# Performance work log

Measured on AMD Instinct MI355X. Metric: run time of the kernel, lower is better.

## Reference

```python
import jax, jax.numpy as jnp
import numpy as np
from jax import lax

D_MODEL = 1024
D_FF = 4096
NUM_EXPERTS = 24
TOP_K = 2
B, S = 2, 2048


def setup_inputs() -> dict:
    key = jax.random.key(0)
    ks = jax.random.split(key, 5)
    x = jax.random.normal(ks[0], (B, S, D_MODEL), dtype=jnp.float32)
    gate_w = jax.random.normal(ks[1], (D_MODEL, NUM_EXPERTS), dtype=jnp.float32) * 0.02
    gate_b = jnp.zeros((NUM_EXPERTS,), dtype=jnp.float32)
    w1 = jax.random.normal(ks[2], (NUM_EXPERTS, D_MODEL, D_FF), dtype=jnp.float32) * 0.02
    b1 = jnp.zeros((NUM_EXPERTS, D_FF), dtype=jnp.float32)
    w2 = jax.random.normal(ks[3], (NUM_EXPERTS, D_FF, D_MODEL), dtype=jnp.float32) * 0.02
    b2 = jnp.zeros((NUM_EXPERTS, D_MODEL), dtype=jnp.float32)
    return {"x": x, "gate_w": gate_w, "gate_b": gate_b,
            "w1": w1, "b1": b1, "w2": w2, "b2": b2}


def reference(x, gate_w, gate_b, w1, b1, w2, b2):
    b, s, d = x.shape
    t = b * s
    xf = x.reshape(t, d)  # [T, d]
    scores = xf @ gate_w + gate_b  # [T, E]
    top_val, top_idx = lax.top_k(scores, TOP_K)  # [T, k]
    prob = jax.nn.softmax(top_val, axis=-1)  # softmax over the top-k logits
    # scatter top-k probabilities into dense per-expert combine weights [T, E]
    combine = jnp.zeros((t, NUM_EXPERTS), dtype=x.dtype)
    combine = combine.at[jnp.arange(t)[:, None], top_idx].add(prob)

    def body(acc, expert):
        w1e, b1e, w2e, b2e, ce = expert  # ce: [T]
        h = jax.nn.gelu(xf @ w1e + b1e, approximate=False)  # exact GELU as torch default
        y = h @ w2e + b2e  # [T, d]
        return acc + ce[:, None] * y, None

    out, _ = lax.scan(body, jnp.zeros_like(xf), (w1, b1, w2, b2, combine.T))
    return out.reshape(b, s, d)
```

## Files before the change

kernel.cpp:

```cpp
#include <hip/hip_runtime.h>
#include <math.h>

#define DM 1024
#define DF 4096
#define NE 24
#define T_TOK 4096
#define T2 (T_TOK*2)

#define BM 128
#define BN 128
#define BK 64
#define MTILES 8
#define NK1 (DM / BK)
#define NK2H (DF / BK / 2)

typedef __attribute__((ext_vector_type(4))) float f32x4;
typedef __attribute__((ext_vector_type(2))) float f32x2;
typedef __attribute__((ext_vector_type(8))) short s16x8;

static __device__ __forceinline__ unsigned short f2bf(float f) {
    unsigned int u = __float_as_uint(f);
    unsigned int r = u + 0x7fffu + ((u >> 16) & 1u);
    return (unsigned short)(r >> 16);
}

static __device__ __forceinline__ unsigned int cvtpk(float lo, float hi) {
    unsigned int r;
    asm("v_cvt_pk_bf16_f32 %0, %1, %2" : "=v"(r) : "v"(lo), "v"(hi));
    return r;
}

#define GLL(gsrc, ldst)                                                          \
    __builtin_amdgcn_global_load_lds(                                            \
        (const __attribute__((address_space(1))) void*)(gsrc),                   \
        (__attribute__((address_space(3))) void*)(ldst), 16, 0, 0)


__global__ void k_transpose_gw(const float* __restrict__ gw, float* __restrict__ gwT) {
    int e = blockIdx.x;
    for (int d = threadIdx.x; d < DM; d += blockDim.x)
        gwT[e * DM + d] = gw[d * NE + e];
}

__global__ void k_gate(const float* __restrict__ x, const float* __restrict__ gwT,
                       const float* __restrict__ gb,
                       int* __restrict__ idx, float* __restrict__ prob) {
    int wave = threadIdx.x >> 6;
    int lane = threadIdx.x & 63;
    int t = blockIdx.x * 4 + wave;
    if (t >= T_TOK) return;
    const float* xr = x + (size_t)t * DM;
    float acc[NE];
#pragma unroll
    for (int e = 0; e < NE; e++) acc[e] = 0.f;
    for (int i = 0; i < DM / 64; i++) {
        int d = lane + i * 64;
        float xv = xr[d];
#pragma unroll
        for (int e = 0; e < NE; e++) acc[e] = fmaf(xv, gwT[e * DM + d], acc[e]);
    }
#pragma unroll
    for (int e = 0; e < NE; e++) {
        float v = acc[e];
        for (int off = 32; off >= 1; off >>= 1) v += __shfl_xor(v, off);
        acc[e] = v;
    }
    if (lane == 0) {
        float v1 = -1e30f, v2 = -1e30f;
        int i1 = -1, i2 = -1;
        for (int e = 0; e < NE; e++) {
            float s = acc[e] + gb[e];
            if (s > v1) { v2 = v1; i2 = i1; v1 = s; i1 = e; }
            else if (s > v2) { v2 = s; i2 = e; }
        }
        float e2 = expf(v2 - v1);
        float inv = 1.f / (1.f + e2);
        idx[t * 2] = i1; idx[t * 2 + 1] = i2;
        prob[t * 2] = inv; prob[t * 2 + 1] = e2 * inv;
    }
}


__global__ __launch_bounds__(1024)
void k_route(const int* __restrict__ idx, int* __restrict__ counts,
             int* __restrict__ offsets, int* __restrict__ slot_tok,
             int* __restrict__ pair_slot) {
    __shared__ int cnt[NE], offs[NE], cur[NE];
    const int tid = threadIdx.x;
    if (tid < NE) cnt[tid] = 0;
    __syncthreads();
    for (int i = tid; i < T2; i += 1024) atomicAdd(&cnt[idx[i]], 1);
    __syncthreads();
    if (tid == 0) {
        int s = 0;
        for (int e = 0; e < NE; e++) {
            offs[e] = s; offsets[e] = s; counts[e] = cnt[e]; s += cnt[e];
        }
    }
    if (tid < NE) cur[tid] = 0;
    __syncthreads();
    for (int i = tid; i < T2; i += 1024) {
        int e = idx[i];
        int pos = offs[e] + atomicAdd(&cur[e], 1);
        slot_tok[pos] = i >> 1;
        pair_slot[i] = pos;
    }
}

__global__ void k_gather(const float* __restrict__ x, const int* __restrict__ slot_tok,
                         unsigned short* __restrict__ Xg) {
    int s = blockIdx.x;
    int tok = slot_tok[s];
    const float4* src = (const float4*)(x + (size_t)tok * DM);
    ushort4* dst = (ushort4*)(Xg + (size_t)s * DM);
    for (int i = threadIdx.x; i < DM / 4; i += blockDim.x) {
        float4 v = src[i];
        ushort4 o;
        o.x = f2bf(v.x); o.y = f2bf(v.y); o.z = f2bf(v.z); o.w = f2bf(v.w);
        dst[i] = o;
    }
}

__global__ void k_combine(const float* __restrict__ Y1, const float* __restrict__ Y2,
                          const int* __restrict__ pair_slot,
                          const float* __restrict__ prob, const int* __restrict__ idx,
                          const float* __restrict__ b2, float* __restrict__ out) {
    int t = blockIdx.x;
    int s1 = pair_slot[t * 2], s2 = pair_slot[t * 2 + 1];
    int e1 = idx[t * 2], e2 = idx[t * 2 + 1];
    float p1 = prob[t * 2], p2 = prob[t * 2 + 1];
    const float4* y1a = (const float4*)(Y1 + (size_t)s1 * DM);
    const float4* y1b = (const float4*)(Y2 + (size_t)s1 * DM);
    const float4* y2a = (const float4*)(Y1 + (size_t)s2 * DM);
    const float4* y2b = (const float4*)(Y2 + (size_t)s2 * DM);
    const float4* ba = (const float4*)(b2 + (size_t)e1 * DM);
    const float4* bb = (const float4*)(b2 + (size_t)e2 * DM);
    float4* o = (float4*)(out + (size_t)t * DM);
    int i = threadIdx.x;
    float4 a0 = y1a[i], a1 = y1b[i], b0 = y2a[i], b1 = y2b[i];
    float4 c = ba[i], d = bb[i];
    float4 r;
    r.x = p1 * (a0.x + a1.x + c.x) + p2 * (b0.x + b1.x + d.x);
    r.y = p1 * (a0.y + a1.y + c.y) + p2 * (b0.y + b1.y + d.y);
    r.z = p1 * (a0.z + a1.z + c.z) + p2 * (b0.z + b1.z + d.z);
    r.w = p1 * (a0.w + a1.w + c.w) + p2 * (b0.w + b1.w + d.w);
    o[i] = r;
}


__global__ __launch_bounds__(512)
void k_mm1(const unsigned short* __restrict__ Xg, const float* __restrict__ w1,
           const float* __restrict__ b1, const int* __restrict__ counts,
           const int* __restrict__ offsets, unsigned short* __restrict__ H) {
    const int TOT = NE * MTILES * (DF / BN);
    int work = (blockIdx.x & 7) * (TOT >> 3) + (blockIdx.x >> 3);
    const int mt = work % MTILES;
    const int en = work / MTILES;
    const int e  = en >> 5;
    const int n0 = (en & 31) * BN;
    const int ne = counts[e];
    const int m0 = mt * BM;
    if (m0 >= ne) return;
    const int rows = min(BM, ne - m0);
    const int slotbase = offsets[e] + m0;

    __shared__ unsigned short As[2][BM * BK];
    __shared__ unsigned short Bs[BN * BK];

    const int tid  = threadIdx.x;
    const int lane = tid & 63;
    const int w    = tid >> 6;
    const int wm   = w >> 1, wn = w & 1;

    const float* w1e = w1 + (size_t)e * DM * DF;
    const int arow = lane >> 3;
    const int gchunk = ((lane & 7) ^ arow) * 8;

    const int swz0 = ((lane >> 4) ^ (lane & 7)) << 4;
    const int swz1 = ((4 | (lane >> 4)) ^ (lane & 7)) << 4;
    const char* Arow0 = (const char*)As[0] + (wm * 32 + (lane & 15)) * 128;
    const char* Arow1 = (const char*)As[1] + (wm * 32 + (lane & 15)) * 128;
    const char* Brow  = (const char*)Bs + (wn * 64 + (lane & 15)) * 128;

    const int np = (tid & 63) * 2;
    const int ckw = w;
    char* BsW0 = (char*)Bs + (np + 0) * 128 + ((ckw ^ ((np + 0) & 7)) << 4);
    char* BsW1 = (char*)Bs + (np + 1) * 128 + ((ckw ^ ((np + 1) & 7)) << 4);

    f32x4 acc[2][4];
#pragma unroll
    for (int a = 0; a < 2; a++)
#pragma unroll
        for (int b = 0; b < 4; b++) acc[a][b] = (f32x4)0.f;

    f32x2 L[8];
    auto loadB = [&](int k0) {
#pragma unroll
        for (int j = 0; j < 8; j++)
            L[j] = *(const f32x2*)(w1e + (size_t)(k0 + w * 8 + j) * DF + n0 + np);
    };
    auto stageA = [&](int buf, int k0) {
#pragma unroll
        for (int q = 0; q < 2; q++) {
            int row = (w * 2 + q) * 8 + arow;
            GLL(Xg + (size_t)(slotbase + row) * DM + k0 + gchunk,
                &As[buf][(w * 2 + q) * 512]);
        }
    };

    stageA(0, 0);
    loadB(0);
#pragma unroll 1
    for (int kt = 0; kt < NK1; ++kt) {
        const int cur = kt & 1;
        __syncthreads();
        if (kt + 1 < NK1) stageA(cur ^ 1, (kt + 1) * BK);
        {
            uint4 v0, v1;
            v0.x = cvtpk(L[0][0], L[1][0]);
            v0.y = cvtpk(L[2][0], L[3][0]);
            v0.z = cvtpk(L[4][0], L[5][0]);
            v0.w = cvtpk(L[6][0], L[7][0]);
            v1.x = cvtpk(L[0][1], L[1][1]);
            v1.y = cvtpk(L[2][1], L[3][1]);
            v1.z = cvtpk(L[4][1], L[5][1]);
            v1.w = cvtpk(L[6][1], L[7][1]);
            *(uint4*)BsW0 = v0;
            *(uint4*)BsW1 = v1;
        }
        if (kt + 1 < NK1) loadB((kt + 1) * BK);
        const char* Arow = cur ? Arow1 : Arow0;
        s16x8 af[2][2];
#pragma unroll
        for (int f = 0; f < 2; f++) {
            af[0][f] = *(const s16x8*)(Arow + f * 2048 + swz0);
            af[1][f] = *(const s16x8*)(Arow + f * 2048 + swz1);
        }
        asm volatile("s_waitcnt lgkmcnt(0)" ::: "memory");
        __builtin_amdgcn_s_barrier();
        __builtin_amdgcn_sched_barrier(0);
        s16x8 bfr[2][4];
#pragma unroll
        for (int f = 0; f < 4; f++) {
            bfr[0][f] = *(const s16x8*)(Brow + f * 2048 + swz0);
            bfr[1][f] = *(const s16x8*)(Brow + f * 2048 + swz1);
        }
#pragma unroll
        for (int ks = 0; ks < 2; ks++)
#pragma unroll
            for (int fm = 0; fm < 2; fm++)
#pragma unroll
                for (int fn = 0; fn < 4; fn++)
                    acc[fm][fn] = __builtin_amdgcn_mfma_f32_16x16x32_bf16(
                        af[ks][fm], bfr[ks][fn], acc[fm][fn], 0, 0, 0);
    }

    const float* b1e = b1 + (size_t)e * DF;
#pragma unroll
    for (int fm = 0; fm < 2; fm++) {
        const int mrow = wm * 32 + fm * 16 + ((lane >> 4) << 2);
#pragma unroll
        for (int fn = 0; fn < 4; fn++) {
            const int ncol = n0 + wn * 64 + fn * 16 + (lane & 15);
            const float bb = b1e[ncol];
#pragma unroll
            for (int r = 0; r < 4; r++) {
                const int m = mrow + r;
                if (m < rows) {
                    float h = acc[fm][fn][r] + bb;
                    h = 0.5f * h * (1.f + erff(h * 0.70710678118654752f));
                    H[(size_t)(slotbase + m) * DF + ncol] = f2bf(h);
                }
            }
        }
    }
}

__global__ __launch_bounds__(512)
void k_mm2(const unsigned short* __restrict__ Hb, const float* __restrict__ w2,
           const int* __restrict__ counts, const int* __restrict__ offsets,
           float* __restrict__ Y1, float* __restrict__ Y2) {
    const int TOT = NE * MTILES * (DM / BN) * 2;
    int work = (blockIdx.x & 7) * (TOT >> 3) + (blockIdx.x >> 3);
    const int mt = work % MTILES;
    int rest = work / MTILES;
    const int ksl = rest & 1;
    const int en = rest >> 1;
    const int e  = en >> 3;
    const int n0 = (en & 7) * BN;
    const int ne = counts[e];
    const int m0 = mt * BM;
    if (m0 >= ne) return;
    const int rows = min(BM, ne - m0);
    const int slotbase = offsets[e] + m0;
    const int kbeg = ksl * (DF / 2);
    float* Y = ksl ? Y2 : Y1;

    __shared__ unsigned short As[2][BM * BK];
    __shared__ unsigned short Bs[BN * BK];

    const int tid  = threadIdx.x;
    const int lane = tid & 63;
    const int w    = tid >> 6;
    const int wm   = w >> 1, wn = w & 1;

    const float* w2e = w2 + (size_t)e * DF * DM;
    const int arow = lane >> 3;
    const int gchunk = ((lane & 7) ^ arow) * 8;

    const int swz0 = ((lane >> 4) ^ (lane & 7)) << 4;
    const int swz1 = ((4 | (lane >> 4)) ^ (lane & 7)) << 4;
    const char* Arow0 = (const char*)As[0] + (wm * 32 + (lane & 15)) * 128;
    const char* Arow1 = (const char*)As[1] + (wm * 32 + (lane & 15)) * 128;
    const char* Brow  = (const char*)Bs + (wn * 64 + (lane & 15)) * 128;

    const int np = (tid & 63) * 2;
    const int ckw = w;
    char* BsW0 = (char*)Bs + (np + 0) * 128 + ((ckw ^ ((np + 0) & 7)) << 4);
    char* BsW1 = (char*)Bs + (np + 1) * 128 + ((ckw ^ ((np + 1) & 7)) << 4);

    f32x4 acc[2][4];
#pragma unroll
    for (int a = 0; a < 2; a++)
#pragma unroll
        for (int b = 0; b < 4; b++) acc[a][b] = (f32x4)0.f;

    f32x2 L[8];
    auto loadB = [&](int k0) {
#pragma unroll
        for (int j = 0; j < 8; j++)
            L[j] = *(const f32x2*)(w2e + (size_t)(k0 + w * 8 + j) * DM + n0 + np);
    };
    auto stageA = [&](int buf, int k0) {
#pragma unroll
        for (int q = 0; q < 2; q++) {
            int row = (w * 2 + q) * 8 + arow;
            GLL(Hb + (size_t)(slotbase + row) * DF + k0 + gchunk,
                &As[buf][(w * 2 + q) * 512]);
        }
    };

    stageA(0, kbeg);
    loadB(kbeg);
#pragma unroll 1
    for (int kt = 0; kt < NK2H; ++kt) {
        const int cur = kt & 1;
        __syncthreads();
        if (kt + 1 < NK2H) stageA(cur ^ 1, kbeg + (kt + 1) * BK);
        {
            uint4 v0, v1;
            v0.x = cvtpk(L[0][0], L[1][0]);
            v0.y = cvtpk(L[2][0], L[3][0]);
            v0.z = cvtpk(L[4][0], L[5][0]);
            v0.w = cvtpk(L[6][0], L[7][0]);
            v1.x = cvtpk(L[0][1], L[1][1]);
            v1.y = cvtpk(L[2][1], L[3][1]);
            v1.z = cvtpk(L[4][1], L[5][1]);
            v1.w = cvtpk(L[6][1], L[7][1]);
            *(uint4*)BsW0 = v0;
            *(uint4*)BsW1 = v1;
        }
        if (kt + 1 < NK2H) loadB(kbeg + (kt + 1) * BK);
        const char* Arow = cur ? Arow1 : Arow0;
        s16x8 af[2][2];
#pragma unroll
        for (int f = 0; f < 2; f++) {
            af[0][f] = *(const s16x8*)(Arow + f * 2048 + swz0);
            af[1][f] = *(const s16x8*)(Arow + f * 2048 + swz1);
        }
        asm volatile("s_waitcnt lgkmcnt(0)" ::: "memory");
        __builtin_amdgcn_s_barrier();
        __builtin_amdgcn_sched_barrier(0);
        s16x8 bfr[2][4];
#pragma unroll
        for (int f = 0; f < 4; f++) {
            bfr[0][f] = *(const s16x8*)(Brow + f * 2048 + swz0);
            bfr[1][f] = *(const s16x8*)(Brow + f * 2048 + swz1);
        }
#pragma unroll
        for (int ks = 0; ks < 2; ks++)
#pragma unroll
            for (int fm = 0; fm < 2; fm++)
#pragma unroll
                for (int fn = 0; fn < 4; fn++)
                    acc[fm][fn] = __builtin_amdgcn_mfma_f32_16x16x32_bf16(
                        af[ks][fm], bfr[ks][fn], acc[fm][fn], 0, 0, 0);
    }

#pragma unroll
    for (int fm = 0; fm < 2; fm++) {
        const int mrow = wm * 32 + fm * 16 + ((lane >> 4) << 2);
#pragma unroll
        for (int fn = 0; fn < 4; fn++) {
            const int ncol = n0 + wn * 64 + fn * 16 + (lane & 15);
#pragma unroll
            for (int r = 0; r < 4; r++) {
                const int m = mrow + r;
                if (m < rows)
                    Y[(size_t)(slotbase + m) * DM + ncol] = acc[fm][fn][r];
            }
        }
    }
}


extern "C" void kernel_launch(void* const* d_in, const int* in_sizes, int n_in,
                              void* d_out, int out_size, void* d_ws, size_t ws_size,
                              hipStream_t stream) {
    const float* x   = (const float*)d_in[0];
    const float* gw  = (const float*)d_in[1];
    const float* gb  = (const float*)d_in[2];
    const float* w1  = (const float*)d_in[3];
    const float* b1  = (const float*)d_in[4];
    const float* w2  = (const float*)d_in[5];
    const float* b2  = (const float*)d_in[6];
    float* out = (float*)d_out;

    size_t off = 0;
    auto alloc = [&](size_t bytes) {
        void* p = (char*)d_ws + off;
        off += (bytes + 255) & ~(size_t)255;
        return p;
    };
    float* gwT       = (float*)alloc(NE * DM * sizeof(float));
    int*   idx       = (int*)alloc(T2 * sizeof(int));
    float* prob      = (float*)alloc(T2 * sizeof(float));
    int*   counts    = (int*)alloc(32 * sizeof(int));
    int*   offsets   = (int*)alloc(32 * sizeof(int));
    int*   slot_tok  = (int*)alloc(T2 * sizeof(int));
    int*   pair_slot = (int*)alloc(T2 * sizeof(int));
    unsigned short* Xg = (unsigned short*)alloc((size_t)(T2 + BM) * DM * sizeof(unsigned short));
    unsigned short* Hb = (unsigned short*)alloc((size_t)(T2 + BM) * DF * sizeof(unsigned short));
    float* Yb        = (float*)alloc((size_t)(T2 + BM) * DM * sizeof(float));
    float* Yb2       = (float*)alloc((size_t)(T2 + BM) * DM * sizeof(float));

    k_transpose_gw<<<NE, 256, 0, stream>>>(gw, gwT);
    k_gate<<<T_TOK / 4, 256, 0, stream>>>(x, gwT, gb, idx, prob);
    k_route<<<1, 1024, 0, stream>>>(idx, counts, offsets, slot_tok, pair_slot);
    k_gather<<<T2, 256, 0, stream>>>(x, slot_tok, Xg);

    k_mm1<<<NE * MTILES * (DF / BN), 512, 0, stream>>>(Xg, w1, b1, counts, offsets, Hb);
    k_mm2<<<NE * MTILES * (DM / BN) * 2, 512, 0, stream>>>(Hb, w2, counts, offsets, Yb, Yb2);
    k_combine<<<T_TOK, 256, 0, stream>>>(Yb, Yb2, pair_slot, prob, idx, b2, out);
}
```

Baseline: 519.2 us.

## Use compact tile map and persistent grid for expert GEMMs

The router now emits a list of occupied (expert, m-tile) pairs and their count. Both GEMM kernels launch a fixed grid of 768 blocks, each looping over a contiguous chunk of work items, instead of launching every possible tile and returning early on empty ones. This is meant to remove the cost of scheduling thousands of idle blocks. The trade-off is possible load imbalance and a different tile ordering, which may change L2 reuse of weights.

```diff
diff --git a/kernel.cpp b/kernel.cpp
--- a/kernel.cpp
+++ b/kernel.cpp
@@ -10,9 +10,9 @@
 #define BM 128
 #define BN 128
 #define BK 64
-#define MTILES 8
 #define NK1 (DM / BK)
 #define NK2H (DF / BK / 2)
+#define PBLK 768
 
 typedef __attribute__((ext_vector_type(4))) float f32x4;
 typedef __attribute__((ext_vector_type(2))) float f32x2;
@@ -84,7 +84,8 @@
 __global__ __launch_bounds__(1024)
 void k_route(const int* __restrict__ idx, int* __restrict__ counts,
              int* __restrict__ offsets, int* __restrict__ slot_tok,
-             int* __restrict__ pair_slot) {
+             int* __restrict__ pair_slot, int* __restrict__ tmap,
+             int* __restrict__ ntiles) {
     __shared__ int cnt[NE], offs[NE], cur[NE];
     const int tid = threadIdx.x;
     if (tid < NE) cnt[tid] = 0;
@@ -92,10 +93,12 @@
     for (int i = tid; i < T2; i += 1024) atomicAdd(&cnt[idx[i]], 1);
     __syncthreads();
     if (tid == 0) {
-        int s = 0;
+        int s = 0, nt = 0;
         for (int e = 0; e < NE; e++) {
             offs[e] = s; offsets[e] = s; counts[e] = cnt[e]; s += cnt[e];
-        }
+            for (int mt = 0; mt * BM < cnt[e]; mt++) tmap[nt++] = (e << 8) | mt;
+        }
+        ntiles[0] = nt;
     }
     if (tid < NE) cur[tid] = 0;
     __syncthreads();
@@ -151,19 +154,8 @@
 __global__ __launch_bounds__(512)
 void k_mm1(const unsigned short* __restrict__ Xg, const float* __restrict__ w1,
            const float* __restrict__ b1, const int* __restrict__ counts,
-           const int* __restrict__ offsets, unsigned short* __restrict__ H) {
-    const int TOT = NE * MTILES * (DF / BN);
-    int work = (blockIdx.x & 7) * (TOT >> 3) + (blockIdx.x >> 3);
-    const int mt = work % MTILES;
-    const int en = work / MTILES;
-    const int e  = en >> 5;
-    const int n0 = (en & 31) * BN;
-    const int ne = counts[e];
-    const int m0 = mt * BM;
-    if (m0 >= ne) return;
-    const int rows = min(BM, ne - m0);
-    const int slotbase = offsets[e] + m0;
-
+           const int* __restrict__ offsets, const int* __restrict__ tmap,
+           const int* __restrict__ ntiles, unsigned short* __restrict__ H) {
     __shared__ unsigned short As[2][BM * BK];
     __shared__ unsigned short Bs[BN * BK];
 
@@ -172,10 +164,8 @@
     const int w    = tid >> 6;
     const int wm   = w >> 1, wn = w & 1;
 
-    const float* w1e = w1 + (size_t)e * DM * DF;
     const int arow = lane >> 3;
     const int gchunk = ((lane & 7) ^ arow) * 8;
-
     const int swz0 = ((lane >> 4) ^ (lane & 7)) << 4;
     const int swz1 = ((4 | (lane >> 4)) ^ (lane & 7)) << 4;
     const char* Arow0 = (const char*)As[0] + (wm * 32 + (lane & 15)) * 128;
@@ -187,89 +177,108 @@
     char* BsW0 = (char*)Bs + (np + 0) * 128 + ((ckw ^ ((np + 0) & 7)) << 4);
     char* BsW1 = (char*)Bs + (np + 1) * 128 + ((ckw ^ ((np + 1) & 7)) << 4);
 
-    f32x4 acc[2][4];
-#pragma unroll
-    for (int a = 0; a < 2; a++)
-#pragma unroll
-        for (int b = 0; b < 4; b++) acc[a][b] = (f32x4)0.f;
-
-    f32x2 L[8];
-    auto loadB = [&](int k0) {
-#pragma unroll
-        for (int j = 0; j < 8; j++)
-            L[j] = *(const f32x2*)(w1e + (size_t)(k0 + w * 8 + j) * DF + n0 + np);
-    };
-    auto stageA = [&](int buf, int k0) {
-#pragma unroll
-        for (int q = 0; q < 2; q++) {
-            int row = (w * 2 + q) * 8 + arow;
-            GLL(Xg + (size_t)(slotbase + row) * DM + k0 + gchunk,
-                &As[buf][(w * 2 + q) * 512]);
-        }
-    };
-
-    stageA(0, 0);
-    loadB(0);
+    const int NT = ntiles[0];
+    const int TOTW = NT * 32;
+    const int CS = (TOTW + PBLK - 1) / PBLK;
+    const int i0 = blockIdx.x * CS;
+    const int i1 = min(i0 + CS, TOTW);
+
 #pragma unroll 1
-    for (int kt = 0; kt < NK1; ++kt) {
-        const int cur = kt & 1;
-        __syncthreads();
-        if (kt + 1 < NK1) stageA(cur ^ 1, (kt + 1) * BK);
-        {
-            uint4 v0, v1;
-            v0.x = cvtpk(L[0][0], L[1][0]);
-            v0.y = cvtpk(L[2][0], L[3][0]);
-            v0.z = cvtpk(L[4][0], L[5][0]);
-            v0.w = cvtpk(L[6][0], L[7][0]);
-            v1.x = cvtpk(L[0][1], L[1][1]);
-            v1.y = cvtpk(L[2][1], L[3][1]);
-            v1.z = cvtpk(L[4][1], L[5][1]);
-            v1.w = cvtpk(L[6][1], L[7][1]);
-            *(uint4*)BsW0 = v0;
-            *(uint4*)BsW1 = v1;
-        }
-        if (kt + 1 < NK1) loadB((kt + 1) * BK);
-        const char* Arow = cur ? Arow1 : Arow0;
-        s16x8 af[2][2];
-#pragma unroll
-        for (int f = 0; f < 2; f++) {
-            af[0][f] = *(const s16x8*)(Arow + f * 2048 + swz0);
-            af[1][f] = *(const s16x8*)(Arow + f * 2048 + swz1);
-        }
-        asm volatile("s_waitcnt lgkmcnt(0)" ::: "memory");
-        __builtin_amdgcn_s_barrier();
-        __builtin_amdgcn_sched_barrier(0);
-        s16x8 bfr[2][4];
-#pragma unroll
-        for (int f = 0; f < 4; f++) {
-            bfr[0][f] = *(const s16x8*)(Brow + f * 2048 + swz0);
-            bfr[1][f] = *(const s16x8*)(Brow + f * 2048 + swz1);
-        }
-#pragma unroll
-        for (int ks = 0; ks < 2; ks++)
-#pragma unroll
-            for (int fm = 0; fm < 2; fm++)
-#pragma unroll
-                for (int fn = 0; fn < 4; fn++)
-                    acc[fm][fn] = __builtin_amdgcn_mfma_f32_16x16x32_bf16(
-                        af[ks][fm], bfr[ks][fn], acc[fm][fn], 0, 0, 0);
-    }
-
-    const float* b1e = b1 + (size_t)e * DF;
-#pragma unroll
-    for (int fm = 0; fm < 2; fm++) {
-        const int mrow = wm * 32 + fm * 16 + ((lane >> 4) << 2);
-#pragma unroll
-        for (int fn = 0; fn < 4; fn++) {
-            const int ncol = n0 + wn * 64 + fn * 16 + (lane & 15);
-            const float bb = b1e[ncol];
-#pragma unroll
-            for (int r = 0; r < 4; r++) {
-                const int m = mrow + r;
-                if (m < rows) {
-                    float h = acc[fm][fn][r] + bb;
-                    h = 0.5f * h * (1.f + erff(h * 0.70710678118654752f));
-                    H[(size_t)(slotbase + m) * DF + ncol] = f2bf(h);
+    for (int item = i0; item < i1; ++item) {
+        const int ti = item % NT;
+        const int n0 = (item / NT) * BN;
+        const int tm = tmap[ti];
+        const int e = tm >> 8, mt = tm & 255;
+        const int ne = counts[e];
+        const int m0 = mt * BM;
+        const int rows = min(BM, ne - m0);
+        const int slotbase = offsets[e] + m0;
+        const float* w1e = w1 + (size_t)e * DM * DF;
+
+        f32x4 acc[2][4];
+#pragma unroll
+        for (int a = 0; a < 2; a++)
+#pragma unroll
+            for (int b = 0; b < 4; b++) acc[a][b] = (f32x4)0.f;
+
+        f32x2 L[8];
+        auto loadB = [&](int k0) {
+#pragma unroll
+            for (int j = 0; j < 8; j++)
+                L[j] = *(const f32x2*)(w1e + (size_t)(k0 + w * 8 + j) * DF + n0 + np);
+        };
+        auto stageA = [&](int buf, int k0) {
+#pragma unroll
+            for (int q = 0; q < 2; q++) {
+                int row = (w * 2 + q) * 8 + arow;
+                GLL(Xg + (size_t)(slotbase + row) * DM + k0 + gchunk,
+                    &As[buf][(w * 2 + q) * 512]);
+            }
+        };
+
+        stageA(0, 0);
+        loadB(0);
+#pragma unroll 1
+        for (int kt = 0; kt < NK1; ++kt) {
+            const int cur = kt & 1;
+            __syncthreads();
+            if (kt + 1 < NK1) stageA(cur ^ 1, (kt + 1) * BK);
+            {
+                uint4 v0, v1;
+                v0.x = cvtpk(L[0][0], L[1][0]);
+                v0.y = cvtpk(L[2][0], L[3][0]);
+                v0.z = cvtpk(L[4][0], L[5][0]);
+                v0.w = cvtpk(L[6][0], L[7][0]);
+                v1.x = cvtpk(L[0][1], L[1][1]);
+                v1.y = cvtpk(L[2][1], L[3][1]);
+                v1.z = cvtpk(L[4][1], L[5][1]);
+                v1.w = cvtpk(L[6][1], L[7][1]);
+                *(uint4*)BsW0 = v0;
+                *(uint4*)BsW1 = v1;
+            }
+            if (kt + 1 < NK1) loadB((kt + 1) * BK);
+            const char* Arow = cur ? Arow1 : Arow0;
+            s16x8 af[2][2];
+#pragma unroll
+            for (int f = 0; f < 2; f++) {
+                af[0][f] = *(const s16x8*)(Arow + f * 2048 + swz0);
+                af[1][f] = *(const s16x8*)(Arow + f * 2048 + swz1);
+            }
+            asm volatile("s_waitcnt lgkmcnt(0)" ::: "memory");
+            __builtin_amdgcn_s_barrier();
+            __builtin_amdgcn_sched_barrier(0);
+            s16x8 bfr[2][4];
+#pragma unroll
+            for (int f = 0; f < 4; f++) {
+                bfr[0][f] = *(const s16x8*)(Brow + f * 2048 + swz0);
+                bfr[1][f] = *(const s16x8*)(Brow + f * 2048 + swz1);
+            }
+#pragma unroll
+            for (int ks = 0; ks < 2; ks++)
+#pragma unroll
+                for (int fm = 0; fm < 2; fm++)
+#pragma unroll
+                    for (int fn = 0; fn < 4; fn++)
+                        acc[fm][fn] = __builtin_amdgcn_mfma_f32_16x16x32_bf16(
+                            af[ks][fm], bfr[ks][fn], acc[fm][fn], 0, 0, 0);
+        }
+
+        const float* b1e = b1 + (size_t)e * DF;
+#pragma unroll
+        for (int fm = 0; fm < 2; fm++) {
+            const int mrow = wm * 32 + fm * 16 + ((lane >> 4) << 2);
+#pragma unroll
+            for (int fn = 0; fn < 4; fn++) {
+                const int ncol = n0 + wn * 64 + fn * 16 + (lane & 15);
+                const float bb = b1e[ncol];
+#pragma unroll
+                for (int r = 0; r < 4; r++) {
+                    const int m = mrow + r;
+                    if (m < rows) {
+                        float h = acc[fm][fn][r] + bb;
+                        h = 0.5f * h * (1.f + erff(h * 0.70710678118654752f));
+                        H[(size_t)(slotbase + m) * DF + ncol] = f2bf(h);
+                    }
                 }
             }
         }
@@ -279,23 +288,8 @@
 __global__ __launch_bounds__(512)
 void k_mm2(const unsigned short* __restrict__ Hb, const float* __restrict__ w2,
            const int* __restrict__ counts, const int* __restrict__ offsets,
+           const int* __restrict__ tmap, const int* __restrict__ ntiles,
            float* __restrict__ Y1, float* __restrict__ Y2) {
-    const int TOT = NE * MTILES * (DM / BN) * 2;
-    int work = (blockIdx.x & 7) * (TOT >> 3) + (blockIdx.x >> 3);
-    const int mt = work % MTILES;
-    int rest = work / MTILES;
-    const int ksl = rest & 1;
-    const int en = rest >> 1;
-    const int e  = en >> 3;
-    const int n0 = (en & 7) * BN;
-    const int ne = counts[e];
-    const int m0 = mt * BM;
-    if (m0 >= ne) return;
-    const int rows = min(BM, ne - m0);
-    const int slotbase = offsets[e] + m0;
-    const int kbeg = ksl * (DF / 2);
-    float* Y = ksl ? Y2 : Y1;
-
     __shared__ unsigned short As[2][BM * BK];
     __shared__ unsigned short Bs[BN * BK];
 
@@ -304,10 +298,8 @@
     const int w    = tid >> 6;
     const int wm   = w >> 1, wn = w & 1;
 
-    const float* w2e = w2 + (size_t)e * DF * DM;
     const int arow = lane >> 3;
     const int gchunk = ((lane & 7) ^ arow) * 8;
-
     const int swz0 = ((lane >> 4) ^ (lane & 7)) << 4;
     const int swz1 = ((4 | (lane >> 4)) ^ (lane & 7)) << 4;
     const char* Arow0 = (const char*)As[0] + (wm * 32 + (lane & 15)) * 128;
@@ -319,85 +311,108 @@
     char* BsW0 = (char*)Bs + (np + 0) * 128 + ((ckw ^ ((np + 0) & 7)) << 4);
     char* BsW1 = (char*)Bs + (np + 1) * 128 + ((ckw ^ ((np + 1) & 7)) << 4);
 
-    f32x4 acc[2][4];
-#pragma unroll
-    for (int a = 0; a < 2; a++)
-#pragma unroll
-        for (int b = 0; b < 4; b++) acc[a][b] = (f32x4)0.f;
-
-    f32x2 L[8];
-    auto loadB = [&](int k0) {
-#pragma unroll
-        for (int j = 0; j < 8; j++)
-            L[j] = *(const f32x2*)(w2e + (size_t)(k0 + w * 8 + j) * DM + n0 + np);
-    };
-    auto stageA = [&](int buf, int k0) {
-#pragma unroll
-        for (int q = 0; q < 2; q++) {
-            int row = (w * 2 + q) * 8 + arow;
-            GLL(Hb + (size_t)(slotbase + row) * DF + k0 + gchunk,
-                &As[buf][(w * 2 + q) * 512]);
-        }
-    };
-
-    stageA(0, kbeg);
-    loadB(kbeg);
+    const int NT = ntiles[0];
+    const int TOTW = NT * 16;
+    const int CS = (TOTW + PBLK - 1) / PBLK;
+    const int i0 = blockIdx.x * CS;
+    const int i1 = min(i0 + CS, TOTW);
+
 #pragma unroll 1
-    for (int kt = 0; kt < NK2H; ++kt) {
-        const int cur = kt & 1;
-        __syncthreads();
-        if (kt + 1 < NK2H) stageA(cur ^ 1, kbeg + (kt + 1) * BK);
-        {
-            uint4 v0, v1;
-            v0.x = cvtpk(L[0][0], L[1][0]);
-            v0.y = cvtpk(L[2][0], L[3][0]);
-            v0.z = cvtpk(L[4][0], L[5][0]);
-            v0.w = cvtpk(L[6][0], L[7][0]);
-            v1.x = cvtpk(L[0][1], L[1][1]);
-            v1.y = cvtpk(L[2][1], L[3][1]);
-            v1.z = cvtpk(L[4][1], L[5][1]);
-            v1.w = cvtpk(L[6][1], L[7][1]);
-            *(uint4*)BsW0 = v0;
-            *(uint4*)BsW1 = v1;
-        }
-        if (kt + 1 < NK2H) loadB(kbeg + (kt + 1) * BK);
-        const char* Arow = cur ? Arow1 : Arow0;
-        s16x8 af[2][2];
-#pragma unroll
-        for (int f = 0; f < 2; f++) {
-            af[0][f] = *(const s16x8*)(Arow + f * 2048 + swz0);
-            af[1][f] = *(const s16x8*)(Arow + f * 2048 + swz1);
-        }
-        asm volatile("s_waitcnt lgkmcnt(0)" ::: "memory");
-        __builtin_amdgcn_s_barrier();
-        __builtin_amdgcn_sched_barrier(0);
-        s16x8 bfr[2][4];
-#pragma unroll
-        for (int f = 0; f < 4; f++) {
-            bfr[0][f] = *(const s16x8*)(Brow + f * 2048 + swz0);
-            bfr[1][f] = *(const s16x8*)(Brow + f * 2048 + swz1);
-        }
-#pragma unroll
-        for (int ks = 0; ks < 2; ks++)
-#pragma unroll
-            for (int fm = 0; fm < 2; fm++)
-#pragma unroll
-                for (int fn = 0; fn < 4; fn++)
-                    acc[fm][fn] = __builtin_amdgcn_mfma_f32_16x16x32_bf16(
-                        af[ks][fm], bfr[ks][fn], acc[fm][fn], 0, 0, 0);
-    }
-
-#pragma unroll
-    for (int fm = 0; fm < 2; fm++) {
-        const int mrow = wm * 32 + fm * 16 + ((lane >> 4) << 2);
-#pragma unroll
-        for (int fn = 0; fn < 4; fn++) {
-            const int ncol = n0 + wn * 64 + fn * 16 + (lane & 15);
-#pragma unroll
-            for (int r = 0; r < 4; r++) {
-                const int m = mrow + r;
-                if (m < rows)
-                    Y[(size_t)(slotbase + m) * DM + ncol] = acc[fm][fn][r];
+    for (int item = i0; item < i1; ++item) {
+        const int ti = item % NT;
+        const int r2 = item / NT;
+        const int ksl = r2 & 1;
+        const int n0 = (r2 >> 1) * BN;
+        const int tm = tmap[ti];
+        const int e = tm >> 8, mt = tm & 255;
+        const int ne = counts[e];
+        const int m0 = mt * BM;
+        const int rows = min(BM, ne - m0);
+        const int slotbase = offsets[e] + m0;
+        const int kbeg = ksl * (DF / 2);
+        float* Y = ksl ? Y2 : Y1;
+        const float* w2e = w2 + (size_t)e * DF * DM;
+
+        f32x4 acc[2][4];
+#pragma unroll
+        for (int a = 0; a < 2; a++)
+#pragma unroll
+            for (int b = 0; b < 4; b++) acc[a][b] = (f32x4)0.f;
+
+        f32x2 L[8];
+        auto loadB = [&](int k0) {
+#pragma unroll
+            for (int j = 0; j < 8; j++)
+                L[j] = *(const f32x2*)(w2e + (size_t)(k0 + w * 8 + j) * DM + n0 + np);
+        };
+        auto stageA = [&](int buf, int k0) {
+#pragma unroll
+            for (int q = 0; q < 2; q++) {
+                int row = (w * 2 + q) * 8 + arow;
+                GLL(Hb + (size_t)(slotbase + row) * DF + k0 + gchunk,
+                    &As[buf][(w * 2 + q) * 512]);
+            }
+        };
+
+        stageA(0, kbeg);
+        loadB(kbeg);
+#pragma unroll 1
+        for (int kt = 0; kt < NK2H; ++kt) {
+            const int cur = kt & 1;
+            __syncthreads();
+            if (kt + 1 < NK2H) stageA(cur ^ 1, kbeg + (kt + 1) * BK);
+            {
+                uint4 v0, v1;
+                v0.x = cvtpk(L[0][0], L[1][0]);
+                v0.y = cvtpk(L[2][0], L[3][0]);
+                v0.z = cvtpk(L[4][0], L[5][0]);
+                v0.w = cvtpk(L[6][0], L[7][0]);
+                v1.x = cvtpk(L[0][1], L[1][1]);
+                v1.y = cvtpk(L[2][1], L[3][1]);
+                v1.z = cvtpk(L[4][1], L[5][1]);
+                v1.w = cvtpk(L[6][1], L[7][1]);
+                *(uint4*)BsW0 = v0;
+                *(uint4*)BsW1 = v1;
+            }
+            if (kt + 1 < NK2H) loadB(kbeg + (kt + 1) * BK);
+            const char* Arow = cur ? Arow1 : Arow0;
+            s16x8 af[2][2];
+#pragma unroll
+            for (int f = 0; f < 2; f++) {
+                af[0][f] = *(const s16x8*)(Arow + f * 2048 + swz0);
+                af[1][f] = *(const s16x8*)(Arow + f * 2048 + swz1);
+            }
+            asm volatile("s_waitcnt lgkmcnt(0)" ::: "memory");
+            __builtin_amdgcn_s_barrier();
+            __builtin_amdgcn_sched_barrier(0);
+            s16x8 bfr[2][4];
+#pragma unroll
+            for (int f = 0; f < 4; f++) {
+                bfr[0][f] = *(const s16x8*)(Brow + f * 2048 + swz0);
+                bfr[1][f] = *(const s16x8*)(Brow + f * 2048 + swz1);
+            }
+#pragma unroll
+            for (int ks = 0; ks < 2; ks++)
+#pragma unroll
+                for (int fm = 0; fm < 2; fm++)
+#pragma unroll
+                    for (int fn = 0; fn < 4; fn++)
+                        acc[fm][fn] = __builtin_amdgcn_mfma_f32_16x16x32_bf16(
+                            af[ks][fm], bfr[ks][fn], acc[fm][fn], 0, 0, 0);
+        }
+
+#pragma unroll
+        for (int fm = 0; fm < 2; fm++) {
+            const int mrow = wm * 32 + fm * 16 + ((lane >> 4) << 2);
+#pragma unroll
+            for (int fn = 0; fn < 4; fn++) {
+                const int ncol = n0 + wn * 64 + fn * 16 + (lane & 15);
+#pragma unroll
+                for (int r = 0; r < 4; r++) {
+                    const int m = mrow + r;
+                    if (m < rows)
+                        Y[(size_t)(slotbase + m) * DM + ncol] = acc[fm][fn][r];
+                }
             }
         }
     }
@@ -429,6 +444,8 @@
     int*   offsets   = (int*)alloc(32 * sizeof(int));
     int*   slot_tok  = (int*)alloc(T2 * sizeof(int));
     int*   pair_slot = (int*)alloc(T2 * sizeof(int));
+    int*   tmap      = (int*)alloc(128 * sizeof(int));
+    int*   ntiles    = (int*)alloc(32 * sizeof(int));
     unsigned short* Xg = (unsigned short*)alloc((size_t)(T2 + BM) * DM * sizeof(unsigned short));
     unsigned short* Hb = (unsigned short*)alloc((size_t)(T2 + BM) * DF * sizeof(unsigned short));
     float* Yb        = (float*)alloc((size_t)(T2 + BM) * DM * sizeof(float));
@@ -436,10 +453,10 @@
 
     k_transpose_gw<<<NE, 256, 0, stream>>>(gw, gwT);
     k_gate<<<T_TOK / 4, 256, 0, stream>>>(x, gwT, gb, idx, prob);
-    k_route<<<1, 1024, 0, stream>>>(idx, counts, offsets, slot_tok, pair_slot);
+    k_route<<<1, 1024, 0, stream>>>(idx, counts, offsets, slot_tok, pair_slot, tmap, ntiles);
     k_gather<<<T2, 256, 0, stream>>>(x, slot_tok, Xg);
 
-    k_mm1<<<NE * MTILES * (DF / BN), 512, 0, stream>>>(Xg, w1, b1, counts, offsets, Hb);
-    k_mm2<<<NE * MTILES * (DM / BN) * 2, 512, 0, stream>>>(Hb, w2, counts, offsets, Yb, Yb2);
+    k_mm1<<<PBLK, 512, 0, stream>>>(Xg, w1, b1, counts, offsets, tmap, ntiles, Hb);
+    k_mm2<<<PBLK, 512, 0, stream>>>(Hb, w2, counts, offsets, tmap, ntiles, Yb, Yb2);
     k_combine<<<T_TOK, 256, 0, stream>>>(Yb, Yb2, pair_slot, prob, idx, b2, out);
 }
```

New measurement: 615.6 us. 1.19x slower.
